# Optimization experiments

Hardware: AMD Instinct MI355X
Metric: run time of the kernel (lower is better)

Reference implementation:

```python
import jax, jax.numpy as jnp
import numpy as np

N_TOKENS = 4096
N_EMBD = 1024
N_EXPERTS = 8
TOP_K = 2
TEMPERATURE = 1.0
PARAM_SCALE = 0.02


def setup_inputs() -> dict:
    key = jax.random.key(0)
    ks = jax.random.split(key, 6)
    x = jax.random.normal(ks[0], (N_TOKENS, N_EMBD), dtype=jnp.float32)
    gate_w = jax.random.normal(ks[1], (N_EMBD, N_EXPERTS), dtype=jnp.float32) * PARAM_SCALE
    w1 = jax.random.normal(ks[2], (N_EXPERTS, N_EMBD, 4 * N_EMBD), dtype=jnp.float32) * PARAM_SCALE
    b1 = jax.random.normal(ks[3], (N_EXPERTS, 4 * N_EMBD), dtype=jnp.float32) * PARAM_SCALE
    w2 = jax.random.normal(ks[4], (N_EXPERTS, 4 * N_EMBD, N_EMBD), dtype=jnp.float32) * PARAM_SCALE
    b2 = jax.random.normal(ks[5], (N_EXPERTS, N_EMBD), dtype=jnp.float32) * PARAM_SCALE
    return {"x": x, "gate_w": gate_w, "w1": w1, "b1": b1, "w2": w2, "b2": b2}


def reference(x, gate_w, w1, b1, w2, b2):
    # Gating: softmax with temperature, top-2, renormalize over the top-2.
    gate_logits = x @ gate_w                              # [N, E]
    gate_probs = jax.nn.softmax(gate_logits / TEMPERATURE, axis=-1)
    top_v, top_i = jax.lax.top_k(gate_probs, TOP_K)       # [N, k]
    top_v = top_v / jnp.sum(top_v, axis=-1, keepdims=True)
    # Per-expert combine weight: sum of renormalized top-k probs routed to e.
    one_hot = jax.nn.one_hot(top_i, N_EXPERTS, dtype=x.dtype)   # [N, k, E]
    combine = jnp.einsum('nk,nke->ne', top_v, one_hot)          # [N, E]
    # Dense expert evaluation (faithful math; loop over fixed small expert set).
    out = jnp.zeros_like(x)
    for e in range(N_EXPERTS):
        h = jax.nn.gelu(x @ w1[e] + b1[e], approximate=False)   # [N, 4C]
        y = h @ w2[e] + b2[e]                                   # [N, C]
        out = out + combine[:, e:e + 1] * y
    return out
```

## Files before the change

kernel.cpp:

```cpp
#include <hip/hip_runtime.h>
#include <math.h>

#define TOKENS 4096
#define EMBD   1024
#define HID    4096
#define NE     8
#define SLOTC  8320

typedef __attribute__((ext_vector_type(8))) short short8;
typedef __attribute__((ext_vector_type(4))) float f32x4;

#define GLOBAL_PTR(p) ((const __attribute__((address_space(1))) void*)(p))
#define LDS_PTR(p)    ((__attribute__((address_space(3))) void*)(p))

__device__ __forceinline__ unsigned short f2bf(float f) {
  unsigned int u = __float_as_uint(f);
  u += 0x7FFFu + ((u >> 16) & 1u);
  return (unsigned short)(u >> 16);
}
__device__ __forceinline__ float bf2f(unsigned short h) {
  return __uint_as_float((unsigned int)h << 16);
}

__device__ __forceinline__ float fast_gelu(float v) {
  float u = fabsf(v) * 0.70710678118654752f;
  float t = 1.0f / (1.0f + 0.3275911f * u);
  float poly = ((((1.061405429f * t - 1.453152027f) * t + 1.421413741f) * t
                 - 0.284496736f) * t + 0.254829592f) * t;
  float erf_abs = 1.0f - poly * __expf(-u * u);
  float er = (v < 0.0f) ? -erf_abs : erf_abs;
  return 0.5f * v * (1.0f + er);
}

__global__ __launch_bounds__(256) void k_gate_cvt(const float* __restrict__ x,
                                                  const float* __restrict__ gw,
                                                  unsigned short* __restrict__ xb,
                                                  int* __restrict__ idx2,
                                                  float* __restrict__ wv) {
  int wave = threadIdx.x >> 6, lane = threadIdx.x & 63;
  int t = blockIdx.x * 4 + wave;
  const float4* xr = (const float4*)(x + (size_t)t * EMBD);
  ushort4* xbr = (ushort4*)(xb + (size_t)t * EMBD);
  float acc[NE];
#pragma unroll
  for (int e = 0; e < NE; e++) acc[e] = 0.f;
#pragma unroll
  for (int ch = 0; ch < 4; ch++) {
    int i = ch * 64 + lane;
    float4 v = xr[i];
    ushort4 o;
    o.x = f2bf(v.x); o.y = f2bf(v.y); o.z = f2bf(v.z); o.w = f2bf(v.w);
    xbr[i] = o;
    int c = i * 4;
    const float* g0 = gw + (size_t)c * NE;
#pragma unroll
    for (int e = 0; e < NE; e++) acc[e] += v.x * g0[e];
#pragma unroll
    for (int e = 0; e < NE; e++) acc[e] += v.y * g0[NE + e];
#pragma unroll
    for (int e = 0; e < NE; e++) acc[e] += v.z * g0[2 * NE + e];
#pragma unroll
    for (int e = 0; e < NE; e++) acc[e] += v.w * g0[3 * NE + e];
  }
#pragma unroll
  for (int e = 0; e < NE; e++) {
#pragma unroll
    for (int off = 32; off > 0; off >>= 1) acc[e] += __shfl_down(acc[e], off);
  }
  if (lane == 0) {
    float best = -1e30f, second = -1e30f;
    int bi = 0, si = 0;
#pragma unroll
    for (int e = 0; e < NE; e++) {
      float l = acc[e];
      if (l > best) { second = best; si = bi; best = l; bi = e; }
      else if (l > second) { second = l; si = e; }
    }
    float b = expf(second - best);
    float w0 = 1.f / (1.f + b);
    float w1 = b / (1.f + b);
    idx2[2 * t] = bi; idx2[2 * t + 1] = si;
    wv[2 * t] = w0; wv[2 * t + 1] = w1;
  }
}

__global__ __launch_bounds__(256) void k_count(const int* __restrict__ idx2,
                                               int* __restrict__ ctrl) {
  __shared__ int cnt[NE];
  int tid = threadIdx.x;
  if (tid < NE) cnt[tid] = 0;
  __syncthreads();
  for (int i = tid; i < TOKENS * 2; i += 256) atomicAdd(&cnt[idx2[i]], 1);
  __syncthreads();
  if (tid == 0) {
    int off = 0;
#pragma unroll
    for (int e = 0; e < NE; e++) { int c = cnt[e]; ctrl[e] = c; ctrl[8 + e] = off; off += c; }
    ctrl[16] = off;
  }
  if (tid < NE) ctrl[17 + tid] = 0;
}

__global__ __launch_bounds__(256) void k_assign(const int* __restrict__ idx2,
                                                int* __restrict__ ctrl,
                                                int* __restrict__ token_list,
                                                int* __restrict__ tok2slot) {
  __shared__ int lpos[NE];
  __shared__ int lbase[NE];
  int tid = threadIdx.x;
  int t = blockIdx.x * 256 + tid;
  if (tid < NE) lpos[tid] = 0;
  __syncthreads();
  int e0 = idx2[2 * t], e1 = idx2[2 * t + 1];
  int p0 = atomicAdd(&lpos[e0], 1);
  int p1 = atomicAdd(&lpos[e1], 1);
  __syncthreads();
  if (tid < NE) lbase[tid] = atomicAdd(&ctrl[17 + tid], lpos[tid]);
  __syncthreads();
  int s0 = ctrl[8 + e0] + lbase[e0] + p0;
  int s1 = ctrl[8 + e1] + lbase[e1] + p1;
  token_list[s0] = t;
  token_list[s1] = t;
  tok2slot[2 * t] = s0;
  tok2slot[2 * t + 1] = s1;
}

__global__ __launch_bounds__(256) void k_trans(const float* __restrict__ in,
                                               unsigned short* __restrict__ out,
                                               int R, int C) {
  __shared__ unsigned short T[64 * 66];
  int e = blockIdx.z;
  const float* ine = in + (size_t)e * R * C;
  unsigned short* oute = out + (size_t)e * R * C;
  int r0 = blockIdx.y * 64;
  int c0 = blockIdx.x * 64;
  int tid = threadIdx.x;
  {
    int c4 = tid & 15;
    int rb = tid >> 4;
#pragma unroll
    for (int it = 0; it < 4; it++) {
      int r = rb + 16 * it;
      float4 v = *(const float4*)(ine + (size_t)(r0 + r) * C + c0 + 4 * c4);
      T[(4 * c4 + 0) * 66 + r] = f2bf(v.x);
      T[(4 * c4 + 1) * 66 + r] = f2bf(v.y);
      T[(4 * c4 + 2) * 66 + r] = f2bf(v.z);
      T[(4 * c4 + 3) * 66 + r] = f2bf(v.w);
    }
  }
  __syncthreads();
  {
    int rr = tid & 7;
    int cq = tid >> 3;
#pragma unroll
    for (int it = 0; it < 2; it++) {
      int c = cq + 32 * it;
      short8 o;
#pragma unroll
      for (int k = 0; k < 8; k++) o[k] = (short)T[c * 66 + 8 * rr + k];
      *(short8*)(oute + (size_t)(c0 + c) * R + r0 + 8 * rr) = o;
    }
  }
}


#define STAGE_G(sA0_, sA1_, sB0_, sB1_, kk, sl) do {                                              \
    __builtin_amdgcn_global_load_lds(GLOBAL_PTR((sA0_) + (kk)), LDS_PTR(lds + (sl) * 16384 + wave * 2048), 16, 0, 0);          \
    __builtin_amdgcn_global_load_lds(GLOBAL_PTR((sA1_) + (kk)), LDS_PTR(lds + (sl) * 16384 + wave * 2048 + 1024), 16, 0, 0);   \
    __builtin_amdgcn_global_load_lds(GLOBAL_PTR((sB0_) + (kk)), LDS_PTR(lds + 65536 + (sl) * 16384 + wave * 2048), 16, 0, 0);  \
    __builtin_amdgcn_global_load_lds(GLOBAL_PTR((sB1_) + (kk)), LDS_PTR(lds + 65536 + (sl) * 16384 + wave * 2048 + 1024), 16, 0, 0); \
  } while (0)

#define STEP_BODY(sl) do {                                                                        \
    const short8* Ap = (const short8*)(lds + (sl) * 16384 + aoff);                                \
    const short8* Bp = (const short8*)(lds + 65536 + (sl) * 16384 + boff);                        \
    short8 af[8], bfr[4];                                                                         \
    _Pragma("unroll")                                                                             \
    for (int f = 0; f < 8; f++) af[f] = Ap[f * 64];                                               \
    _Pragma("unroll")                                                                             \
    for (int n = 0; n < 4; n++) bfr[n] = Bp[n * 64];                                              \
    __builtin_amdgcn_s_setprio(1);                                                                \
    _Pragma("unroll")                                                                             \
    for (int f = 0; f < 8; f++)                                                                   \
      _Pragma("unroll")                                                                           \
      for (int n = 0; n < 4; n++)                                                                 \
        acc[f][n] = __builtin_amdgcn_mfma_f32_16x16x32_bf16(af[f], bfr[n], acc[f][n], 0, 0, 0);   \
    __builtin_amdgcn_s_setprio(0);                                                                \
  } while (0)

__global__ __launch_bounds__(512, 2) void k_gemm1(
    const unsigned short* __restrict__ xb,
    const unsigned short* __restrict__ w1t,
    const float* __restrict__ b1,
    const int* __restrict__ ctrl,
    const int* __restrict__ token_list,
    unsigned short* __restrict__ Hbuf) {
  int h = blockIdx.x;
  int e = h & 7;
  int j = h >> 3;
  int m_base = (j & 15) * 256;
  int nb = (j >> 4) * 256;
  int cnt = ctrl[e];
  if (m_base >= cnt) return;
  int off_e = ctrl[8 + e];
  int tid = threadIdx.x;
  int wave = tid >> 6, lane = tid & 63;
  int wr = wave >> 2, wc = wave & 3;
  int q4 = lane >> 4, cc = lane & 15;

  __shared__ __align__(16) char lds[131072];

  int qg = (lane & 3) ^ ((lane >> 3) & 3);
  int row0 = wave * 32 + (lane >> 2);
  int row1 = row0 + 16;
  int tok0 = token_list[off_e + min(m_base + row0, cnt - 1)];
  int tok1 = token_list[off_e + min(m_base + row1, cnt - 1)];
  const unsigned short* sA0 = xb + (size_t)tok0 * EMBD + qg * 8;
  const unsigned short* sA1 = xb + (size_t)tok1 * EMBD + qg * 8;
  const unsigned short* wbp = w1t + (size_t)e * HID * EMBD;
  const unsigned short* sB0 = wbp + (size_t)(nb + row0) * EMBD + qg * 8;
  const unsigned short* sB1 = wbp + (size_t)(nb + row1) * EMBD + qg * 8;

  int swz = (q4 ^ ((cc >> 1) & 3)) * 16;
  int aoff = (wr * 128 + cc) * 64 + swz;
  int boff = (wc * 64 + cc) * 64 + swz;

  f32x4 acc[8][4];
#pragma unroll
  for (int f = 0; f < 8; f++)
#pragma unroll
    for (int n = 0; n < 4; n++) acc[f][n] = (f32x4){0.f, 0.f, 0.f, 0.f};

  STAGE_G(sA0, sA1, sB0, sB1, 0, 0);
  STAGE_G(sA0, sA1, sB0, sB1, 32, 1);
  STAGE_G(sA0, sA1, sB0, sB1, 64, 2);

#pragma unroll 4
  for (int c = 0; c < 32; ++c) {
    asm volatile("s_waitcnt vmcnt(8)" ::: "memory");
    __builtin_amdgcn_s_barrier();
    __builtin_amdgcn_sched_barrier(0);
    int kk = ((c + 3) * 32) & (EMBD - 1);
    STAGE_G(sA0, sA1, sB0, sB1, kk, (c + 3) & 3);
    STEP_BODY(c & 3);
  }
  asm volatile("s_waitcnt vmcnt(0)" ::: "memory");

  const float* b1e = b1 + (size_t)e * HID;
  float bias[4];
#pragma unroll
  for (int n = 0; n < 4; n++) bias[n] = b1e[nb + wc * 64 + n * 16 + cc];
#pragma unroll
  for (int f = 0; f < 8; f++) {
#pragma unroll
    for (int r = 0; r < 4; r++) {
      int m_loc = wr * 128 + f * 16 + q4 * 4 + r;
      int m = m_base + m_loc;
      if (m < cnt) {
        size_t hrow = (size_t)(off_e + m) * HID;
#pragma unroll
        for (int n = 0; n < 4; n++)
          Hbuf[hrow + nb + wc * 64 + n * 16 + cc] = f2bf(fast_gelu(acc[f][n][r] + bias[n]));
      }
    }
  }
}

__global__ __launch_bounds__(512, 2) void k_gemm2(
    const unsigned short* __restrict__ Hbuf,
    const unsigned short* __restrict__ w2t,
    const int* __restrict__ ctrl,
    unsigned short* __restrict__ Yp) {
  int h = blockIdx.x;
  int e = h & 7;
  int s = (h >> 3) & 1;
  int j = h >> 4;
  int m_base = (j & 15) * 256;
  int nb = (j >> 4) * 256;
  int cnt = ctrl[e];
  if (m_base >= cnt) return;
  int off_e = ctrl[8 + e];
  int tid = threadIdx.x;
  int wave = tid >> 6, lane = tid & 63;
  int wr = wave >> 2, wc = wave & 3;
  int q4 = lane >> 4, cc = lane & 15;

  __shared__ __align__(16) char lds[131072];

  int qg = (lane & 3) ^ ((lane >> 3) & 3);
  int row0 = wave * 32 + (lane >> 2);
  int row1 = row0 + 16;
  int ar0 = off_e + min(m_base + row0, cnt - 1);
  int ar1 = off_e + min(m_base + row1, cnt - 1);
  int kbeg = s * (HID / 2);
  const unsigned short* sA0 = Hbuf + (size_t)ar0 * HID + kbeg + qg * 8;
  const unsigned short* sA1 = Hbuf + (size_t)ar1 * HID + kbeg + qg * 8;
  const unsigned short* wbp = w2t + (size_t)e * EMBD * HID;
  const unsigned short* sB0 = wbp + (size_t)(nb + row0) * HID + kbeg + qg * 8;
  const unsigned short* sB1 = wbp + (size_t)(nb + row1) * HID + kbeg + qg * 8;

  int swz = (q4 ^ ((cc >> 1) & 3)) * 16;
  int aoff = (wr * 128 + cc) * 64 + swz;
  int boff = (wc * 64 + cc) * 64 + swz;

  f32x4 acc[8][4];
#pragma unroll
  for (int f = 0; f < 8; f++)
#pragma unroll
    for (int n = 0; n < 4; n++) acc[f][n] = (f32x4){0.f, 0.f, 0.f, 0.f};

  STAGE_G(sA0, sA1, sB0, sB1, 0, 0);
  STAGE_G(sA0, sA1, sB0, sB1, 32, 1);
  STAGE_G(sA0, sA1, sB0, sB1, 64, 2);

#pragma unroll 4
  for (int c = 0; c < 64; ++c) {
    asm volatile("s_waitcnt vmcnt(8)" ::: "memory");
    __builtin_amdgcn_s_barrier();
    __builtin_amdgcn_sched_barrier(0);
    int kk = ((c + 3) * 32) & (HID / 2 - 1);
    STAGE_G(sA0, sA1, sB0, sB1, kk, (c + 3) & 3);
    STEP_BODY(c & 3);
  }
  asm volatile("s_waitcnt vmcnt(0)" ::: "memory");

  unsigned short* Yps = Yp + (size_t)s * SLOTC * EMBD;
#pragma unroll
  for (int f = 0; f < 8; f++) {
#pragma unroll
    for (int r = 0; r < 4; r++) {
      int m_loc = wr * 128 + f * 16 + q4 * 4 + r;
      int m = m_base + m_loc;
      if (m < cnt) {
        size_t yrow = (size_t)(off_e + m) * EMBD;
#pragma unroll
        for (int n = 0; n < 4; n++)
          Yps[yrow + nb + wc * 64 + n * 16 + cc] = f2bf(acc[f][n][r]);
      }
    }
  }
}

__global__ __launch_bounds__(256) void k_combine(const unsigned short* __restrict__ Yp,
                                                 const float* __restrict__ b2,
                                                 const int* __restrict__ idx2,
                                                 const float* __restrict__ wv,
                                                 const int* __restrict__ tok2slot,
                                                 float* __restrict__ out) {
  int t = blockIdx.x;
  int tid = threadIdx.x;
  int c = tid * 4;
  int e0 = idx2[2 * t], e1 = idx2[2 * t + 1];
  float w0 = wv[2 * t], w1 = wv[2 * t + 1];
  int s0 = tok2slot[2 * t], s1 = tok2slot[2 * t + 1];
  ushort4 p00 = *(const ushort4*)(Yp + ((size_t)0 * SLOTC + s0) * EMBD + c);
  ushort4 p01 = *(const ushort4*)(Yp + ((size_t)1 * SLOTC + s0) * EMBD + c);
  ushort4 p10 = *(const ushort4*)(Yp + ((size_t)0 * SLOTC + s1) * EMBD + c);
  ushort4 p11 = *(const ushort4*)(Yp + ((size_t)1 * SLOTC + s1) * EMBD + c);
  float4 b20 = *(const float4*)(b2 + (size_t)e0 * EMBD + c);
  float4 b21 = *(const float4*)(b2 + (size_t)e1 * EMBD + c);
  float4 r;
  r.x = w0 * (bf2f(p00.x) + bf2f(p01.x) + b20.x) + w1 * (bf2f(p10.x) + bf2f(p11.x) + b21.x);
  r.y = w0 * (bf2f(p00.y) + bf2f(p01.y) + b20.y) + w1 * (bf2f(p10.y) + bf2f(p11.y) + b21.y);
  r.z = w0 * (bf2f(p00.z) + bf2f(p01.z) + b20.z) + w1 * (bf2f(p10.z) + bf2f(p11.z) + b21.z);
  r.w = w0 * (bf2f(p00.w) + bf2f(p01.w) + b20.w) + w1 * (bf2f(p10.w) + bf2f(p11.w) + b21.w);
  *(float4*)(out + (size_t)t * EMBD + c) = r;
}

extern "C" void kernel_launch(void* const* d_in, const int* in_sizes, int n_in,
                              void* d_out, int out_size, void* d_ws, size_t ws_size,
                              hipStream_t stream) {
  (void)in_sizes; (void)n_in; (void)out_size; (void)ws_size;
  const float* x      = (const float*)d_in[0];
  const float* gate_w = (const float*)d_in[1];
  const float* w1     = (const float*)d_in[2];
  const float* b1     = (const float*)d_in[3];
  const float* w2     = (const float*)d_in[4];
  const float* b2     = (const float*)d_in[5];
  float* out = (float*)d_out;

  char* ws = (char*)d_ws;
  size_t off = 0;
  auto alloc = [&](size_t bytes) {
    char* p = ws + off;
    off += (bytes + 255) & ~(size_t)255;
    return p;
  };
  unsigned short* xb    = (unsigned short*)alloc((size_t)TOKENS * EMBD * 2);
  unsigned short* w1t   = (unsigned short*)alloc((size_t)NE * HID * EMBD * 2);
  unsigned short* w2t   = (unsigned short*)alloc((size_t)NE * EMBD * HID * 2);
  unsigned short* Hbuf  = (unsigned short*)alloc((size_t)SLOTC * HID * 2);
  unsigned short* Yp    = (unsigned short*)alloc((size_t)2 * SLOTC * EMBD * 2);
  int*   token_list     = (int*)alloc((size_t)SLOTC * 4);
  int*   idx2           = (int*)alloc((size_t)TOKENS * 2 * 4);
  float* wv             = (float*)alloc((size_t)TOKENS * 2 * 4);
  int*   tok2slot       = (int*)alloc((size_t)TOKENS * 2 * 4);
  int*   ctrl           = (int*)alloc(32 * 4);

  k_gate_cvt<<<TOKENS / 4, 256, 0, stream>>>(x, gate_w, xb, idx2, wv);
  k_count<<<1, 256, 0, stream>>>(idx2, ctrl);
  k_assign<<<TOKENS / 256, 256, 0, stream>>>(idx2, ctrl, token_list, tok2slot);
  k_trans<<<dim3(HID / 64, EMBD / 64, NE), 256, 0, stream>>>(w1, w1t, EMBD, HID);
  k_trans<<<dim3(EMBD / 64, HID / 64, NE), 256, 0, stream>>>(w2, w2t, HID, EMBD);
  k_gemm1<<<2048, 512, 0, stream>>>(xb, w1t, b1, ctrl, token_list, Hbuf);
  k_gemm2<<<1024, 512, 0, stream>>>(Hbuf, w2t, ctrl, Yp);
  k_combine<<<TOKENS, 256, 0, stream>>>(Yp, b2, idx2, wv, tok2slot, out);
}
```

Baseline: 601.7 us.

## Split GEMM k-step into two barrier-separated phases interleaving staging with MFMA

Restructures the main loops of both expert GEMM kernels so each k-step runs as two phases, each with half the A fragments. A-tile and B-tile global-to-LDS staging is issued separately inside each phase, and the loop is peeled to drain the pipeline explicitly instead of wrapping around modulo K. The LDS row layout changes so each wave loads 16 rows at a time. The goal is to overlap global loads and LDS reads with MFMA work and cut register pressure from fragments, at the cost of more barriers per k-step.

```diff
diff --git a/kernel.cpp b/kernel.cpp
--- a/kernel.cpp
+++ b/kernel.cpp
@@ -164,29 +164,69 @@
 }
 
 
-#define STAGE_G(sA0_, sA1_, sB0_, sB1_, kk, sl) do {                                              \
-    __builtin_amdgcn_global_load_lds(GLOBAL_PTR((sA0_) + (kk)), LDS_PTR(lds + (sl) * 16384 + wave * 2048), 16, 0, 0);          \
-    __builtin_amdgcn_global_load_lds(GLOBAL_PTR((sA1_) + (kk)), LDS_PTR(lds + (sl) * 16384 + wave * 2048 + 1024), 16, 0, 0);   \
-    __builtin_amdgcn_global_load_lds(GLOBAL_PTR((sB0_) + (kk)), LDS_PTR(lds + 65536 + (sl) * 16384 + wave * 2048), 16, 0, 0);  \
-    __builtin_amdgcn_global_load_lds(GLOBAL_PTR((sB1_) + (kk)), LDS_PTR(lds + 65536 + (sl) * 16384 + wave * 2048 + 1024), 16, 0, 0); \
+#define SB __builtin_amdgcn_sched_barrier(0)
+
+#define STAGE_A(sl, koff) do {                                                                        \
+    __builtin_amdgcn_global_load_lds(GLOBAL_PTR(sA0 + (koff)), LDS_PTR(lds + (sl) * 16384 + wave * 1024), 16, 0, 0);        \
+    __builtin_amdgcn_global_load_lds(GLOBAL_PTR(sA1 + (koff)), LDS_PTR(lds + (sl) * 16384 + 8192 + wave * 1024), 16, 0, 0); \
   } while (0)
-
-#define STEP_BODY(sl) do {                                                                        \
-    const short8* Ap = (const short8*)(lds + (sl) * 16384 + aoff);                                \
-    const short8* Bp = (const short8*)(lds + 65536 + (sl) * 16384 + boff);                        \
-    short8 af[8], bfr[4];                                                                         \
-    _Pragma("unroll")                                                                             \
-    for (int f = 0; f < 8; f++) af[f] = Ap[f * 64];                                               \
-    _Pragma("unroll")                                                                             \
-    for (int n = 0; n < 4; n++) bfr[n] = Bp[n * 64];                                              \
-    __builtin_amdgcn_s_setprio(1);                                                                \
-    _Pragma("unroll")                                                                             \
-    for (int f = 0; f < 8; f++)                                                                   \
-      _Pragma("unroll")                                                                           \
-      for (int n = 0; n < 4; n++)                                                                 \
-        acc[f][n] = __builtin_amdgcn_mfma_f32_16x16x32_bf16(af[f], bfr[n], acc[f][n], 0, 0, 0);   \
-    __builtin_amdgcn_s_setprio(0);                                                                \
+#define STAGE_B(sl, koff) do {                                                                        \
+    __builtin_amdgcn_global_load_lds(GLOBAL_PTR(sB0 + (koff)), LDS_PTR(lds + 65536 + (sl) * 16384 + wave * 1024), 16, 0, 0);        \
+    __builtin_amdgcn_global_load_lds(GLOBAL_PTR(sB1 + (koff)), LDS_PTR(lds + 65536 + (sl) * 16384 + 8192 + wave * 1024), 16, 0, 0); \
   } while (0)
+
+#define PH0(sl, STAGEOP) do {                                                                         \
+    const char* Ab_ = lds + (sl) * 16384;                                                             \
+    const char* Bb_ = lds + 65536 + (sl) * 16384;                                                     \
+    _Pragma("unroll")                                                                                 \
+    for (int f = 0; f < 4; f++) a_[f] = *(const short8*)(Ab_ + aoff + f * 1024);                      \
+    _Pragma("unroll")                                                                                 \
+    for (int n = 0; n < 4; n++) b_[n] = *(const short8*)(Bb_ + boff + n * 1024);                      \
+    STAGEOP;                                                                                          \
+    SB;                                                                                               \
+    __builtin_amdgcn_s_barrier();                                                                     \
+    SB;                                                                                               \
+    asm volatile("s_waitcnt lgkmcnt(0)" ::: "memory");                                                \
+    SB;                                                                                               \
+    __builtin_amdgcn_s_setprio(1);                                                                    \
+    _Pragma("unroll")                                                                                 \
+    for (int f = 0; f < 4; f++)                                                                       \
+      _Pragma("unroll")                                                                               \
+      for (int n = 0; n < 4; n++)                                                                     \
+        acc[f][n] = __builtin_amdgcn_mfma_f32_16x16x32_bf16(a_[f], b_[n], acc[f][n], 0, 0, 0);        \
+    __builtin_amdgcn_s_setprio(0);                                                                    \
+    SB;                                                                                               \
+    __builtin_amdgcn_s_barrier();                                                                     \
+    SB;                                                                                               \
+  } while (0)
+
+#define PH1(sl, STAGEOP, WAITOP) do {                                                                 \
+    const char* Ab_ = lds + (sl) * 16384;                                                             \
+    _Pragma("unroll")                                                                                 \
+    for (int f = 0; f < 4; f++) a_[f] = *(const short8*)(Ab_ + aoff + (f + 4) * 1024);                \
+    STAGEOP;                                                                                          \
+    WAITOP;                                                                                           \
+    SB;                                                                                               \
+    __builtin_amdgcn_s_barrier();                                                                     \
+    SB;                                                                                               \
+    asm volatile("s_waitcnt lgkmcnt(0)" ::: "memory");                                                \
+    SB;                                                                                               \
+    __builtin_amdgcn_s_setprio(1);                                                                    \
+    _Pragma("unroll")                                                                                 \
+    for (int f = 0; f < 4; f++)                                                                       \
+      _Pragma("unroll")                                                                               \
+      for (int n = 0; n < 4; n++)                                                                     \
+        acc[f + 4][n] = __builtin_amdgcn_mfma_f32_16x16x32_bf16(a_[f], b_[n], acc[f + 4][n], 0, 0, 0);\
+    __builtin_amdgcn_s_setprio(0);                                                                    \
+    SB;                                                                                               \
+    __builtin_amdgcn_s_barrier();                                                                     \
+    SB;                                                                                               \
+  } while (0)
+
+#define VM8 asm volatile("s_waitcnt vmcnt(8)" ::: "memory")
+#define VM4 asm volatile("s_waitcnt vmcnt(4)" ::: "memory")
+#define VM0 asm volatile("s_waitcnt vmcnt(0)" ::: "memory")
+#define NOP (void)0
 
 __global__ __launch_bounds__(512, 2) void k_gemm1(
     const unsigned short* __restrict__ xb,
@@ -210,41 +250,46 @@
 
   __shared__ __align__(16) char lds[131072];
 
-  int qg = (lane & 3) ^ ((lane >> 3) & 3);
-  int row0 = wave * 32 + (lane >> 2);
-  int row1 = row0 + 16;
+  int chS = (lane & 3) ^ ((lane >> 3) & 3);
+  int row0 = wave * 16 + (lane >> 2);
+  int row1 = 128 + row0;
   int tok0 = token_list[off_e + min(m_base + row0, cnt - 1)];
   int tok1 = token_list[off_e + min(m_base + row1, cnt - 1)];
-  const unsigned short* sA0 = xb + (size_t)tok0 * EMBD + qg * 8;
-  const unsigned short* sA1 = xb + (size_t)tok1 * EMBD + qg * 8;
+  const unsigned short* sA0 = xb + (size_t)tok0 * EMBD + chS * 8;
+  const unsigned short* sA1 = xb + (size_t)tok1 * EMBD + chS * 8;
   const unsigned short* wbp = w1t + (size_t)e * HID * EMBD;
-  const unsigned short* sB0 = wbp + (size_t)(nb + row0) * EMBD + qg * 8;
-  const unsigned short* sB1 = wbp + (size_t)(nb + row1) * EMBD + qg * 8;
+  const unsigned short* sB0 = wbp + (size_t)(nb + row0) * EMBD + chS * 8;
+  const unsigned short* sB1 = wbp + (size_t)(nb + row1) * EMBD + chS * 8;
 
   int swz = (q4 ^ ((cc >> 1) & 3)) * 16;
-  int aoff = (wr * 128 + cc) * 64 + swz;
-  int boff = (wc * 64 + cc) * 64 + swz;
+  int aoff = wr * 8192 + cc * 64 + swz;
+  int boff = (wc >> 1) * 8192 + (wc & 1) * 4096 + cc * 64 + swz;
 
   f32x4 acc[8][4];
 #pragma unroll
   for (int f = 0; f < 8; f++)
 #pragma unroll
     for (int n = 0; n < 4; n++) acc[f][n] = (f32x4){0.f, 0.f, 0.f, 0.f};
-
-  STAGE_G(sA0, sA1, sB0, sB1, 0, 0);
-  STAGE_G(sA0, sA1, sB0, sB1, 32, 1);
-  STAGE_G(sA0, sA1, sB0, sB1, 64, 2);
+  short8 a_[4], b_[4];
+
+  STAGE_A(0, 0);  STAGE_B(0, 0);
+  STAGE_A(1, 32); STAGE_B(1, 32);
+  STAGE_A(2, 64); STAGE_B(2, 64);
+  VM8;
+  SB;
+  __builtin_amdgcn_s_barrier();
+  SB;
 
 #pragma unroll 4
-  for (int c = 0; c < 32; ++c) {
-    asm volatile("s_waitcnt vmcnt(8)" ::: "memory");
-    __builtin_amdgcn_s_barrier();
-    __builtin_amdgcn_sched_barrier(0);
-    int kk = ((c + 3) * 32) & (EMBD - 1);
-    STAGE_G(sA0, sA1, sB0, sB1, kk, (c + 3) & 3);
-    STEP_BODY(c & 3);
-  }
-  asm volatile("s_waitcnt vmcnt(0)" ::: "memory");
+  for (int kt = 0; kt < 29; ++kt) {
+    int sl = kt & 3, sl3 = (kt + 3) & 3;
+    int koff3 = (kt + 3) * 32;
+    PH0(sl, STAGE_A(sl3, koff3));
+    PH1(sl, STAGE_B(sl3, koff3), VM8);
+  }
+  PH0(1, NOP); PH1(1, NOP, VM4);
+  PH0(2, NOP); PH1(2, NOP, VM0);
+  PH0(3, NOP); PH1(3, NOP, NOP);
 
   const float* b1e = b1 + (size_t)e * HID;
   float bias[4];
@@ -287,42 +332,47 @@
 
   __shared__ __align__(16) char lds[131072];
 
-  int qg = (lane & 3) ^ ((lane >> 3) & 3);
-  int row0 = wave * 32 + (lane >> 2);
-  int row1 = row0 + 16;
+  int chS = (lane & 3) ^ ((lane >> 3) & 3);
+  int row0 = wave * 16 + (lane >> 2);
+  int row1 = 128 + row0;
   int ar0 = off_e + min(m_base + row0, cnt - 1);
   int ar1 = off_e + min(m_base + row1, cnt - 1);
   int kbeg = s * (HID / 2);
-  const unsigned short* sA0 = Hbuf + (size_t)ar0 * HID + kbeg + qg * 8;
-  const unsigned short* sA1 = Hbuf + (size_t)ar1 * HID + kbeg + qg * 8;
+  const unsigned short* sA0 = Hbuf + (size_t)ar0 * HID + kbeg + chS * 8;
+  const unsigned short* sA1 = Hbuf + (size_t)ar1 * HID + kbeg + chS * 8;
   const unsigned short* wbp = w2t + (size_t)e * EMBD * HID;
-  const unsigned short* sB0 = wbp + (size_t)(nb + row0) * HID + kbeg + qg * 8;
-  const unsigned short* sB1 = wbp + (size_t)(nb + row1) * HID + kbeg + qg * 8;
+  const unsigned short* sB0 = wbp + (size_t)(nb + row0) * HID + kbeg + chS * 8;
+  const unsigned short* sB1 = wbp + (size_t)(nb + row1) * HID + kbeg + chS * 8;
 
   int swz = (q4 ^ ((cc >> 1) & 3)) * 16;
-  int aoff = (wr * 128 + cc) * 64 + swz;
-  int boff = (wc * 64 + cc) * 64 + swz;
+  int aoff = wr * 8192 + cc * 64 + swz;
+  int boff = (wc >> 1) * 8192 + (wc & 1) * 4096 + cc * 64 + swz;
 
   f32x4 acc[8][4];
 #pragma unroll
   for (int f = 0; f < 8; f++)
 #pragma unroll
     for (int n = 0; n < 4; n++) acc[f][n] = (f32x4){0.f, 0.f, 0.f, 0.f};
-
-  STAGE_G(sA0, sA1, sB0, sB1, 0, 0);
-  STAGE_G(sA0, sA1, sB0, sB1, 32, 1);
-  STAGE_G(sA0, sA1, sB0, sB1, 64, 2);
+  short8 a_[4], b_[4];
+
+  STAGE_A(0, 0);  STAGE_B(0, 0);
+  STAGE_A(1, 32); STAGE_B(1, 32);
+  STAGE_A(2, 64); STAGE_B(2, 64);
+  VM8;
+  SB;
+  __builtin_amdgcn_s_barrier();
+  SB;
 
 #pragma unroll 4
-  for (int c = 0; c < 64; ++c) {
-    asm volatile("s_waitcnt vmcnt(8)" ::: "memory");
-    __builtin_amdgcn_s_barrier();
-    __builtin_amdgcn_sched_barrier(0);
-    int kk = ((c + 3) * 32) & (HID / 2 - 1);
-    STAGE_G(sA0, sA1, sB0, sB1, kk, (c + 3) & 3);
-    STEP_BODY(c & 3);
-  }
-  asm volatile("s_waitcnt vmcnt(0)" ::: "memory");
+  for (int kt = 0; kt < 61; ++kt) {
+    int sl = kt & 3, sl3 = (kt + 3) & 3;
+    int koff3 = (kt + 3) * 32;
+    PH0(sl, STAGE_A(sl3, koff3));
+    PH1(sl, STAGE_B(sl3, koff3), VM8);
+  }
+  PH0(1, NOP); PH1(1, NOP, VM4);
+  PH0(2, NOP); PH1(2, NOP, VM0);
+  PH0(3, NOP); PH1(3, NOP, NOP);
 
   unsigned short* Yps = Yp + (size_t)s * SLOTC * EMBD;
 #pragma unroll
```

Result: no change. 606.0 us (+0.7%).
